# Optimization experiments

Measured on AMD Instinct MI355X. Metric: run time of the kernel, lower is better.

The kernel has to match this reference:

```python
import jax, jax.numpy as jnp
import numpy as np
from jax import lax

THRESHOLD = 0.5
KERNEL_SIZE = 4

# OpenCV morphologyEx(MORPH_OPEN) = erosion followed by dilation.
# For an even ksize k=4 with default anchor (-1,-1) -> anchor=(2,2):
#   erosion window offsets  = [-2, +1]  -> pad (2, 1)
#   dilation (kernel mirrored) offsets = [-1, +2] -> pad (1, 2)

def _erode(m, k):
    return lax.reduce_window(m, jnp.inf, lax.min,
                             window_dimensions=(1, k, k),
                             window_strides=(1, 1, 1),
                             padding=((0, 0), (k // 2, k - 1 - k // 2), (k // 2, k - 1 - k // 2)))

def _dilate(m, k):
    return lax.reduce_window(m, -jnp.inf, lax.max,
                             window_dimensions=(1, k, k),
                             window_strides=(1, 1, 1),
                             padding=((0, 0), (k - 1 - k // 2, k // 2), (k - 1 - k // 2, k // 2)))

def setup_inputs() -> dict:
    key = jax.random.key(0)
    k1, k2 = jax.random.split(key)
    score = jax.random.uniform(k1, (32, 1000), dtype=jnp.float32)
    mask = jax.random.uniform(k2, (32, 1024, 1024), dtype=jnp.float32)
    return {"score": score, "mask": mask}

def reference(score, mask):
    score = jnp.where(THRESHOLD <= score, score, jnp.zeros((), score.dtype))
    mask = jnp.where(THRESHOLD <= mask, mask, jnp.zeros((), mask.dtype))
    mask = _dilate(_erode(mask, KERNEL_SIZE), KERNEL_SIZE)  # morphological opening
    return (score, mask)
```

## Files before the change

### kernel.cpp

```cpp
#include <hip/hip_runtime.h>
#include <math.h>


#define H 1024
#define W 1024
#define R 16
#define STRIPS (H / R)
#define BATCH 32
#define MASK_BLOCKS (STRIPS * BATCH)
#define N_SCORE 32000
#define SCORE_BLOCKS ((N_SCORE + 255) / 256)
#define ITERS (R + 6)
#define LROW 1032
#define NSLOT 4

__device__ __forceinline__ float th(float v) { return v >= 0.5f ? v : 0.0f; }

__global__ __launch_bounds__(256)
void fused_kernel(const float* __restrict__ score,
                  const float* __restrict__ mask,
                  float* __restrict__ out) {
    const int bid0 = blockIdx.x;
    const int tid  = threadIdx.x;

    if (bid0 < SCORE_BLOCKS) {
        int i = bid0 * 256 + tid;
        if (i < N_SCORE) out[i] = th(score[i]);
        return;
    }
    const int mb0 = bid0 - SCORE_BLOCKS;
    const int bid = (mb0 & 7) * (MASK_BLOCKS / 8) + (mb0 >> 3);

    const int b     = bid >> 6;
    const int strip = bid & 63;
    const int y0    = strip * R;
    const int wave  = tid >> 6;
    const int c0    = tid * 4;

    const float* img  = mask + (size_t)b * (H * W);
    float*       outp = out + N_SCORE + (size_t)b * (H * W);

    __shared__ float smem[NSLOT * LROW];

    if (tid < 8 * NSLOT) {
        int s = tid >> 3, k = tid & 7;
        smem[s * LROW + (k < 4 ? k : 1024 + k)] = INFINITY;
    }
    __syncthreads();

    const bool eL = (tid == 0);
    const bool eR = (tid == 255);

#define STAGE(IT) do {                                                        \
        int t_  = y0 - 3 + (IT);                                              \
        int tc_ = t_ < 0 ? 0 : (t_ > H - 1 ? H - 1 : t_);        \
        const float* gsrc = img + (size_t)tc_ * W + c0;         \
        float* ldst = &smem[((IT) & 3) * LROW + 4 + (wave << 8)];  \
        __builtin_amdgcn_global_load_lds(                                     \
            (const __attribute__((address_space(1))) void*)gsrc,              \
            (__attribute__((address_space(3))) void*)ldst, 16, 0, 0);         \
    } while (0)

    float hmP[7], q1[7], q2[7];
    for (int m = 0; m < 7; ++m) { hmP[m] = q1[m] = q2[m] = INFINITY; }
    float hxP[4], u1[4], u2[4];
    for (int j = 0; j < 4; ++j)  { hxP[j] = u1[j] = u2[j] = -INFINITY; }

    STAGE(0); STAGE(1);

#define STEP(IT) do {                                                         \
        if ((IT) + 2 < ITERS) STAGE((IT) + 2);                                \
        { constexpr int K_ = ((IT) + 1 < ITERS ? 1 : 0)                       \
                           + ((IT) + 2 < ITERS ? 1 : 0)                       \
                           + ((IT) >= 7 ? 1 : 0) + ((IT) >= 8 ? 1 : 0);       \
          asm volatile("s_waitcnt vmcnt(%0)" :: "i"(K_) : "memory"); }        \
        __builtin_amdgcn_s_barrier();                                         \
        __builtin_amdgcn_sched_barrier(0);                                    \
        {                                                                     \
            const int t = y0 - 3 + (IT);                                      \
            const bool rowOK = (t >= 0) && (t < H);              \
            const float* ls = &smem[((IT) & 3) * LROW + c0];                  \
            float4 L0 = *(const float4*)(ls);            \
            float4 L1 = *(const float4*)(ls + 4);        \
            float4 L2 = *(const float4*)(ls + 8);        \
            float ar[10];                                                     \
            ar[0] = L0.y; ar[1] = L0.z; ar[2] = L0.w;                         \
            ar[3] = L1.x; ar[4] = L1.y; ar[5] = L1.z; ar[6] = L1.w;           \
            ar[7] = L2.x; ar[8] = L2.y; ar[9] = L2.z;                         \
            float p[9];                                                       \
            for (int m = 0; m < 9; ++m) p[m] = fminf(ar[m], ar[m + 1]);       \
            float hm[7];                                                      \
            for (int m = 0; m < 7; ++m) {                                     \
                float v = fminf(p[m], p[m + 2]);                              \
                hm[m] = rowOK ? v : INFINITY;            \
            }                                                                 \
            const int r = t - 1;                                              \
            const float rlim = (r >= 0 && r < H) ? INFINITY : -INFINITY;      \
            float qt[7], ec[7];                                               \
            for (int m = 0; m < 7; ++m) {                                     \
                qt[m] = fminf(hmP[m], hm[m]);                                 \
                ec[m] = fminf(fminf(qt[m], q2[m]), rlim);                     \
            }                                                                 \
            ec[0] = eL ? -INFINITY : ec[0];             \
            ec[5] = eR ? -INFINITY : ec[5];             \
            ec[6] = eR ? -INFINITY : ec[6];             \
            for (int m = 0; m < 7; ++m) { q2[m] = q1[m]; q1[m] = qt[m]; hmP[m] = hm[m]; } \
            float p2[6];                                                      \
            for (int j = 0; j < 6; ++j) p2[j] = fmaxf(ec[j], ec[j + 1]);      \
            float hx[4], ur[4];                                               \
            for (int j = 0; j < 4; ++j) {                                     \
                hx[j] = fmaxf(p2[j], p2[j + 2]);                              \
                ur[j] = fmaxf(hxP[j], hx[j]);                                 \
            }                                                                 \
            if ((IT) >= 6) {                                                  \
                const int y = t - 3;                                          \
                float o0 = th(fmaxf(ur[0], u2[0]));                           \
                float o1 = th(fmaxf(ur[1], u2[1]));                           \
                float o2 = th(fmaxf(ur[2], u2[2]));                           \
                float o3 = th(fmaxf(ur[3], u2[3]));                           \
                *(float4*)(outp + (size_t)y * W + c0) =                       \
                    make_float4(o0, o1, o2, o3);                              \
            }                                                                 \
            for (int j = 0; j < 4; ++j) { u2[j] = u1[j]; u1[j] = ur[j]; hxP[j] = hx[j]; } \
        }                                                                     \
    } while (0)

    STEP(0);  STEP(1);  STEP(2);  STEP(3);  STEP(4);  STEP(5);
    STEP(6);  STEP(7);  STEP(8);  STEP(9);  STEP(10); STEP(11);
    STEP(12); STEP(13); STEP(14); STEP(15); STEP(16); STEP(17);
    STEP(18); STEP(19); STEP(20); STEP(21);

#undef STEP
#undef STAGE
}

extern "C" void kernel_launch(void* const* d_in, const int* in_sizes, int n_in,
                              void* d_out, int out_size, void* d_ws, size_t ws_size,
                              hipStream_t stream) {
    const float* score = (const float*)d_in[0];
    const float* mask  = (const float*)d_in[1];
    float* out = (float*)d_out;

    const int grid = MASK_BLOCKS + SCORE_BLOCKS;
    fused_kernel<<<grid, 256, 0, stream>>>(score, mask, out);
}
```

Before: 248.9 us.

## Give each wave a private LDS region with halo loads to drop block barriers

Each wave now stages its own 256-column slice plus left and right halo vectors into a private LDS region, so no wave reads data loaded by another wave. This removes the per-row s_barrier and the shared infinity padding initialization. Image-edge columns are replaced with infinity in registers. The cost is an extra small global-to-LDS load per row for two lanes and a doubled vmcnt accounting; correctness relies on the wave-local waitcnt ordering being sufficient and on the irregular per-lane LDS offsets not causing bank conflicts.

```diff
diff --git a/kernel.cpp b/kernel.cpp
--- a/kernel.cpp
+++ b/kernel.cpp
@@ -11,7 +11,7 @@
 #define N_SCORE 32000
 #define SCORE_BLOCKS ((N_SCORE + 255) / 256)
 #define ITERS (R + 6)
-#define LROW 1032
+#define REGF 264
 #define NSLOT 4
 
 __device__ __forceinline__ float th(float v) { return v >= 0.5f ? v : 0.0f; }
@@ -35,30 +35,36 @@
     const int strip = bid & 63;
     const int y0    = strip * R;
     const int wave  = tid >> 6;
-    const int c0    = tid * 4;
+    const int lane  = tid & 63;
+    const int c0w   = wave << 8;
+    const int c0    = c0w + (lane << 2);
 
     const float* img  = mask + (size_t)b * (H * W);
     float*       outp = out + N_SCORE + (size_t)b * (H * W);
 
-    __shared__ float smem[NSLOT * LROW];
+    __shared__ float smem[NSLOT * 4 * REGF];
 
-    if (tid < 8 * NSLOT) {
-        int s = tid >> 3, k = tid & 7;
-        smem[s * LROW + (k < 4 ? k : 1024 + k)] = INFINITY;
-    }
-    __syncthreads();
-
-    const bool eL = (tid == 0);
-    const bool eR = (tid == 255);
+    const bool eL = (c0 == 0);
+    const bool eR = (c0 == W - 4);
+    const int oH = (lane == 0) ? (c0w > 0 ? c0w - 4 : 0)
+                               : (c0w + 256 < W ? c0w + 256 : W - 4);
+    const int a0 = (lane == 0)  ? 0  : (16 + (lane << 4));
+    const int a1 = 32 + (lane << 4);
+    const int a2 = (lane == 63) ? 16 : (48 + (lane << 4));
 
 #define STAGE(IT) do {                                                        \
         int t_  = y0 - 3 + (IT);                                              \
         int tc_ = t_ < 0 ? 0 : (t_ > H - 1 ? H - 1 : t_);        \
-        const float* gsrc = img + (size_t)tc_ * W + c0;         \
-        float* ldst = &smem[((IT) & 3) * LROW + 4 + (wave << 8)];  \
+        const float* row_ = img + (size_t)tc_ * W;                            \
+        float* rg_ = &smem[((((IT) & 3) << 2) + wave) * REGF];                \
         __builtin_amdgcn_global_load_lds(                                     \
-            (const __attribute__((address_space(1))) void*)gsrc,              \
-            (__attribute__((address_space(3))) void*)ldst, 16, 0, 0);         \
+            (const __attribute__((address_space(1))) void*)(row_ + c0w + (lane << 2)), \
+            (__attribute__((address_space(3))) void*)(rg_ + 8), 16, 0, 0);    \
+        if (lane < 2) {                                                       \
+            __builtin_amdgcn_global_load_lds(                                 \
+                (const __attribute__((address_space(1))) void*)(row_ + oH),   \
+                (__attribute__((address_space(3))) void*)(rg_), 16, 0, 0);    \
+        }                                                                     \
     } while (0)
 
     float hmP[7], q1[7], q2[7];
@@ -70,23 +76,26 @@
 
 #define STEP(IT) do {                                                         \
         if ((IT) + 2 < ITERS) STAGE((IT) + 2);                                \
-        { constexpr int K_ = ((IT) + 1 < ITERS ? 1 : 0)                       \
-                           + ((IT) + 2 < ITERS ? 1 : 0)                       \
+        { constexpr int K_ = 2 * ((((IT)+1) < ITERS ? 1 : 0)                  \
+                                + (((IT)+2) < ITERS ? 1 : 0))                 \
                            + ((IT) >= 7 ? 1 : 0) + ((IT) >= 8 ? 1 : 0);       \
           asm volatile("s_waitcnt vmcnt(%0)" :: "i"(K_) : "memory"); }        \
-        __builtin_amdgcn_s_barrier();                                         \
         __builtin_amdgcn_sched_barrier(0);                                    \
         {                                                                     \
             const int t = y0 - 3 + (IT);                                      \
             const bool rowOK = (t >= 0) && (t < H);              \
-            const float* ls = &smem[((IT) & 3) * LROW + c0];                  \
-            float4 L0 = *(const float4*)(ls);            \
-            float4 L1 = *(const float4*)(ls + 4);        \
-            float4 L2 = *(const float4*)(ls + 8);        \
+            const char* rgc = (const char*)&smem[((((IT) & 3) << 2) + wave) * REGF]; \
+            float4 A0 = *(const float4*)(rgc + a0);      \
+            float4 A1 = *(const float4*)(rgc + a1);      \
+            float4 A2 = *(const float4*)(rgc + a2);      \
             float ar[10];                                                     \
-            ar[0] = L0.y; ar[1] = L0.z; ar[2] = L0.w;                         \
-            ar[3] = L1.x; ar[4] = L1.y; ar[5] = L1.z; ar[6] = L1.w;           \
-            ar[7] = L2.x; ar[8] = L2.y; ar[9] = L2.z;                         \
+            ar[0] = eL ? INFINITY : A0.y;                       \
+            ar[1] = eL ? INFINITY : A0.z;                       \
+            ar[2] = eL ? INFINITY : A0.w;                       \
+            ar[3] = A1.x; ar[4] = A1.y; ar[5] = A1.z; ar[6] = A1.w;           \
+            ar[7] = eR ? INFINITY : A2.x;                       \
+            ar[8] = eR ? INFINITY : A2.y;                       \
+            ar[9] = eR ? INFINITY : A2.z;                       \
             float p[9];                                                       \
             for (int m = 0; m < 9; ++m) p[m] = fminf(ar[m], ar[m + 1]);       \
             float hm[7];                                                      \
@@ -101,9 +110,9 @@
                 qt[m] = fminf(hmP[m], hm[m]);                                 \
                 ec[m] = fminf(fminf(qt[m], q2[m]), rlim);                     \
             }                                                                 \
-            ec[0] = eL ? -INFINITY : ec[0];             \
-            ec[5] = eR ? -INFINITY : ec[5];             \
-            ec[6] = eR ? -INFINITY : ec[6];             \
+            ec[0] = eL ? -INFINITY : ec[0];              \
+            ec[5] = eR ? -INFINITY : ec[5];              \
+            ec[6] = eR ? -INFINITY : ec[6];              \
             for (int m = 0; m < 7; ++m) { q2[m] = q1[m]; q1[m] = qt[m]; hmP[m] = hm[m]; } \
             float p2[6];                                                      \
             for (int j = 0; j < 6; ++j) p2[j] = fmaxf(ec[j], ec[j + 1]);      \
```

New measurement: 251.4 us. No clear change (+1.0%).
